# Optimization experiments

Measured on AMD Instinct MI355X. Metric: run time of the kernel, lower is better.

The kernel has to match this reference:

```python
import jax, jax.numpy as jnp
import numpy as np

B, L, E, H = 2, 2048, 1024, 16
D = E // H  # 64


def setup_inputs() -> dict:
    key = jax.random.key(0)
    ks = jax.random.split(key, 9)
    return {
        "query": jax.random.normal(ks[0], (B, L, E), dtype=jnp.float32),
        "value": jax.random.normal(ks[1], (B, L, E), dtype=jnp.float32),
        "key": jax.random.normal(ks[2], (B, L, E), dtype=jnp.float32),
        "mask": jax.random.randint(ks[3], (B, 1, L, L), 0, 2, dtype=jnp.int32),
        "Wq": jax.random.normal(ks[4], (D, D), dtype=jnp.float32) * 0.05,
        "Wk": jax.random.normal(ks[5], (D, D), dtype=jnp.float32) * 0.05,
        "Wv": jax.random.normal(ks[6], (D, D), dtype=jnp.float32) * 0.05,
        "Wfc": jax.random.normal(ks[7], (E, E), dtype=jnp.float32) * 0.02,
        "bfc": jax.random.normal(ks[8], (E,), dtype=jnp.float32) * 0.02,
    }


def reference(query, value, key, mask, Wq, Wk, Wv, Wfc, bfc):
    b, q_len, _ = query.shape
    k_len = key.shape[1]
    v_len = value.shape[1]
    # split heads: [b, l, H, D]
    q = query.reshape(b, q_len, H, D)
    k = key.reshape(b, k_len, H, D)
    v = value.reshape(b, v_len, H, D)
    # per-head linear projections (shared weights across heads, no bias)
    q = jnp.einsum('bqhd,ed->bqhe', q, Wq)
    k = jnp.einsum('bkhd,ed->bkhe', k, Wk)
    v = jnp.einsum('bvhd,ed->bvhe', v, Wv)
    # attention scores [b, H, q, k]
    attn = jnp.einsum('bqhd,bkhd->bhqk', q, k)
    # NOTE: original masks BEFORE scaling, and scales by sqrt(embedding_size)
    attn = jnp.where(mask == 0, jnp.float32(-1e20), attn)
    attn = attn / jnp.float32(E ** 0.5)
    attn = jax.nn.softmax(attn, axis=3)
    out = jnp.einsum('bhqk,bkhd->bqhd', attn, v).reshape(b, q_len, E)
    out = out @ Wfc.T + bfc
    return out
```

## Files before the change

kernel.cpp:

```cpp
#include <hip/hip_runtime.h>
#include <hip/hip_bf16.h>


#define B_ 2
#define L_ 2048
#define E_ 1024
#define H_ 16
#define D_ 64

typedef __attribute__((ext_vector_type(8))) short s8v;
typedef __attribute__((ext_vector_type(4))) float f4v;

__device__ __forceinline__ f4v mfma16(s8v a, s8v b, f4v c) {
    return __builtin_amdgcn_mfma_f32_16x16x32_bf16(a, b, c, 0, 0, 0);
}

__device__ __forceinline__ float fast_exp2(float x) {
    return __builtin_amdgcn_exp2f(x);
}

__device__ __forceinline__ ushort bf16bits(float f) {
    __hip_bfloat16 h = __float2bfloat16(f);
    return *(ushort*)&h;
}

__device__ __forceinline__ void glds16(const __hip_bfloat16* g, ushort* l) {
    __builtin_amdgcn_global_load_lds(
        (const __attribute__((address_space(1))) void*)g,
        (__attribute__((address_space(3))) void*)l,
        16, 0, 0);
}

__device__ __forceinline__ s8v ld8_dual(const void* p, size_t idx, bool isf32) {
    if (isf32) {
        const float* pf = (const float*)p + idx;
        f4v f0 = *(const f4v*)pf;
        f4v f1 = *(const f4v*)(pf + 4);
        s8v r;
        r[0] = (short)bf16bits(f0[0]); r[1] = (short)bf16bits(f0[1]);
        r[2] = (short)bf16bits(f0[2]); r[3] = (short)bf16bits(f0[3]);
        r[4] = (short)bf16bits(f1[0]); r[5] = (short)bf16bits(f1[1]);
        r[6] = (short)bf16bits(f1[2]); r[7] = (short)bf16bits(f1[3]);
        return r;
    }
    return *(const s8v*)((const __hip_bfloat16*)p + idx);
}

__device__ __forceinline__ s8v ld8_ws(const __hip_bfloat16* p) {
    return *(const s8v*)p;
}

__device__ __forceinline__ void cvt_piece(
    size_t i4, const void* Wfc, const void* bfc,
    __hip_bfloat16* wfc_bf, __hip_bfloat16* bfc_bf, bool isf32)
{
    const size_t base = i4 * 4;
    const size_t n1 = (size_t)E_ * E_;
    if (base >= n1 + E_) return;
    const void* src = (base < n1) ? Wfc : bfc;
    const size_t off = (base < n1) ? base : base - n1;
    __hip_bfloat16* dst = (base < n1) ? (wfc_bf + off) : (bfc_bf + off);
    if (isf32) {
        f4v v = *(const f4v*)((const float*)src + off);
        #pragma unroll
        for (int j = 0; j < 4; ++j) dst[j] = __float2bfloat16(v[j]);
    } else {
        *(ushort4*)dst = *(const ushort4*)((const ushort*)src + off);
    }
}

__global__ void detect_kernel(const ushort* __restrict__ q, int* __restrict__ flag) {
    __shared__ int cnt;
    if (threadIdx.x == 0) cnt = 0;
    __syncthreads();
    int bad = 0;
    #pragma unroll
    for (int i = 0; i < 16; ++i) {
        ushort u = q[threadIdx.x * 16 + i];
        int e = (u >> 7) & 0xFF;
        if (e >= 0x8E) ++bad;
    }
    atomicAdd(&cnt, bad);
    __syncthreads();
    if (threadIdx.x == 0) *flag = (cnt > 100) ? 1 : 0;
}

__global__ __launch_bounds__(256) void proj_all_kernel(
    const void* __restrict__ q_in, const void* __restrict__ k_in,
    const void* __restrict__ v_in,
    const void* __restrict__ Wq, const void* __restrict__ Wk,
    const void* __restrict__ Wv,
    const void* __restrict__ Wfc, const void* __restrict__ bfc,
    const int* __restrict__ mask, unsigned long long* __restrict__ mbits,
    __hip_bfloat16* __restrict__ qp, __hip_bfloat16* __restrict__ kp,
    __hip_bfloat16* __restrict__ vpT,
    __hip_bfloat16* __restrict__ wfc_bf, __hip_bfloat16* __restrict__ bfc_bf,
    const int* __restrict__ flag)
{
    __shared__ __align__(16) ushort tile[64][72];
    const bool isf32 = (*flag != 0);
    const int wave = threadIdx.x >> 6;
    const int lane = threadIdx.x & 63;
    const int quad = lane >> 4;
    const int l16  = lane & 15;

    if (blockIdx.y == 3) {
        const int lane_ = threadIdx.x & 63;
        const size_t wbase = (size_t)blockIdx.x * 128 + wave * 32;
        #pragma unroll 4
        for (int i = 0; i < 32; ++i) {
            const size_t widx = wbase + i;
            const int v = mask[widx * 64 + lane_];
            const unsigned long long bal = __ballot(v != 0);
            if (lane_ == 0) mbits[widx] = bal;
        }
        return;
    }
    if (blockIdx.y == 4) {
        cvt_piece((size_t)blockIdx.x * 256 + threadIdx.x, Wfc, bfc, wfc_bf, bfc_bf, isf32);
        if (blockIdx.x == 0)
            cvt_piece((size_t)(E_ * (size_t)E_ / 4) + threadIdx.x, Wfc, bfc, wfc_bf, bfc_bf, isf32);
        return;
    }
    if (blockIdx.y < 2) {
        const void* X = blockIdx.y == 0 ? q_in : k_in;
        const void* W = blockIdx.y == 0 ? Wq : Wk;
        __hip_bfloat16* dst = blockIdx.y == 0 ? qp : kp;
        const float oscale = (blockIdx.y == 0) ? 0.045084439755930314f : 1.0f;
        const int m0 = (blockIdx.x * 4 + wave) * 16;

        const size_t abase = (size_t)(m0 + l16) * D_;
        s8v a0 = ld8_dual(X, abase + quad * 8, isf32);
        s8v a1 = ld8_dual(X, abase + 32 + quad * 8, isf32);

        f4v acc[4];
        #pragma unroll
        for (int nt = 0; nt < 4; ++nt) {
            const size_t bbase = (size_t)(nt * 16 + l16) * D_;
            s8v b0 = ld8_dual(W, bbase + quad * 8, isf32);
            s8v b1 = ld8_dual(W, bbase + 32 + quad * 8, isf32);
            f4v c = {0.f, 0.f, 0.f, 0.f};
            c = mfma16(a0, b0, c);
            c = mfma16(a1, b1, c);
            acc[nt] = c;
        }
        #pragma unroll
        for (int r = 0; r < 4; ++r) {
            const int m = m0 + quad * 4 + r;
            const int h = m & 15;
            const int bl = m >> 4;
            const int b = bl >> 11;
            const int l = bl & (L_ - 1);
            #pragma unroll
            for (int nt = 0; nt < 4; ++nt) {
                const int e = nt * 16 + l16;
                dst[(((size_t)(b * H_ + h)) * L_ + l) * D_ + e] =
                    __float2bfloat16(acc[nt][r] * oscale);
            }
        }
    } else {
        const int l0 = (blockIdx.x & 31) * 64;
        const int bh = blockIdx.x >> 5;
        const int b = bh >> 4, h = bh & 15;
        const int lw = l0 + wave * 16;

        const size_t xbase = ((size_t)(b * L_ + lw + l16)) * E_ + h * D_;
        s8v a0 = ld8_dual(v_in, xbase + quad * 8, isf32);
        s8v a1 = ld8_dual(v_in, xbase + 32 + quad * 8, isf32);

        #pragma unroll
        for (int nt = 0; nt < 4; ++nt) {
            const int e = nt * 16 + l16;
            s8v b0 = ld8_dual(Wv, (size_t)e * D_ + quad * 8, isf32);
            s8v b1 = ld8_dual(Wv, (size_t)e * D_ + 32 + quad * 8, isf32);
            f4v c = {0.f, 0.f, 0.f, 0.f};
            c = mfma16(a0, b0, c);
            c = mfma16(a1, b1, c);
            #pragma unroll
            for (int r = 0; r < 4; ++r)
                tile[wave * 16 + quad * 4 + r][e] = bf16bits(c[r]);
        }
        __syncthreads();
        const int e  = threadIdx.x >> 2;
        const int lc = (threadIdx.x & 3) * 16;
        s8v s0, s1;
        #pragma unroll
        for (int i = 0; i < 8; ++i) {
            s0[i] = (short)tile[lc + i][e];
            s1[i] = (short)tile[lc + 8 + i][e];
        }
        __hip_bfloat16* drow = vpT + ((size_t)bh * D_ + e) * L_ + l0 + lc;
        *(s8v*)drow = s0;
        *(s8v*)(drow + 8) = s1;
    }
}

__global__ __launch_bounds__(256) void cvt_wfc_kernel(
    const void* __restrict__ Wfc, const void* __restrict__ bfc,
    __hip_bfloat16* __restrict__ wfc_bf, __hip_bfloat16* __restrict__ bfc_bf,
    const int* __restrict__ flag)
{
    cvt_piece((size_t)blockIdx.x * 256 + threadIdx.x, Wfc, bfc, wfc_bf, bfc_bf, *flag != 0);
}

__global__ __launch_bounds__(256, 4) void attn_kernel(
    const __hip_bfloat16* __restrict__ qp,
    const __hip_bfloat16* __restrict__ kp,
    const __hip_bfloat16* __restrict__ vpT,
    const unsigned long long* __restrict__ mbits,
    __hip_bfloat16* __restrict__ attn_out)
{
    __shared__ __align__(16) ushort kbuf[2][64 * 64];
    __shared__ __align__(16) ushort vbuf[2][64 * 64];
    __shared__ __align__(16) ushort pbuf[4][16 * 64];

    const int wave = threadIdx.x >> 6;
    const int lane = threadIdx.x & 63;
    const int quad = lane >> 4;
    const int l16  = lane & 15;
    const int sw   = l16 & 7;
    const int bh = blockIdx.y;
    const int b = bh >> 4, h = bh & 15;
    const int q0 = blockIdx.x * 64 + wave * 16;

    const uint NEGB = __float_as_uint(-4.5084439e18f);

    const __hip_bfloat16* kbh = kp + (size_t)bh * L_ * D_;
    const __hip_bfloat16* vbh = vpT + (size_t)bh * D_ * L_;
    const unsigned long long* mrow = mbits + ((size_t)b * L_ + q0 + l16) * 32;

    const int lrow = lane >> 3;
    const int lchk = (lane & 7) ^ lrow;
    const int r0 = wave * 16;
    const __hip_bfloat16* kg0 = kbh + (size_t)(r0 + lrow) * D_ + lchk * 8;
    const __hip_bfloat16* kg1 = kbh + (size_t)(r0 + 8 + lrow) * D_ + lchk * 8;
    const __hip_bfloat16* vg0 = vbh + (size_t)(r0 + lrow) * L_ + lchk * 8;
    const __hip_bfloat16* vg1 = vbh + (size_t)(r0 + 8 + lrow) * L_ + lchk * 8;

    const __hip_bfloat16* qbase = qp + ((size_t)bh * L_ + q0) * D_;
    s8v qa0 = ld8_ws(qbase + (size_t)l16 * D_ + quad * 8);
    s8v qa1 = ld8_ws(qbase + (size_t)l16 * D_ + 32 + quad * 8);

    float rsum = 0.f;
    f4v o[4];
    #pragma unroll
    for (int nt = 0; nt < 4; ++nt) o[nt] = (f4v){0.f, 0.f, 0.f, 0.f};

    uint2* pdst[4];
    #pragma unroll
    for (int nt = 0; nt < 4; ++nt) {
        const int c = nt * 2 + (quad >> 1);
        pdst[nt] = (uint2*)&pbuf[wave][l16 * 64 + ((c ^ sw) << 3) + 4 * (quad & 1)];
    }

    glds16(kg0, &kbuf[0][r0 * 64]);
    glds16(kg1, &kbuf[0][r0 * 64 + 512]);
    glds16(vg0, &vbuf[0][r0 * 64]);
    glds16(vg1, &vbuf[0][r0 * 64 + 512]);
    __syncthreads();

    int cur = 0;
    for (int it = 0; it < 32; ++it) {
        const int k0 = it * 64;
        const unsigned long long wq = mrow[it];
        const uint wlo = (uint)wq, whi = (uint)(wq >> 32);
        if (it < 31) {
            glds16(kg0 + (size_t)(k0 + 64) * D_, &kbuf[cur ^ 1][r0 * 64]);
            glds16(kg1 + (size_t)(k0 + 64) * D_, &kbuf[cur ^ 1][r0 * 64 + 512]);
            glds16(vg0 + (k0 + 64), &vbuf[cur ^ 1][r0 * 64]);
            glds16(vg1 + (k0 + 64), &vbuf[cur ^ 1][r0 * 64 + 512]);
        }
        f4v s[4];
        #pragma unroll
        for (int nt = 0; nt < 4; ++nt) {
            const ushort* kr = &kbuf[cur][(nt * 16 + l16) * 64];
            s8v kb0 = *(const s8v*)(kr + ((quad ^ sw) << 3));
            s8v kb1 = *(const s8v*)(kr + (((quad + 4) ^ sw) << 3));
            f4v c = {0.f, 0.f, 0.f, 0.f};
            c = mfma16(kb0, qa0, c);
            c = mfma16(kb1, qa1, c);
            s[nt] = c;
        }
        #pragma unroll
        for (int nt = 0; nt < 4; ++nt) {
            const uint w = (nt & 2) ? whi : wlo;
            float pr[4];
            #pragma unroll
            for (int r = 0; r < 4; ++r) {
                const int idx = ((nt & 1) << 4) + quad * 4 + r;
                const uint m = (uint)(((int)(w << (31 - idx))) >> 31);
                const uint sb = (__float_as_uint(s[nt][r]) & m) | (NEGB & ~m);
                const float p = fast_exp2(__uint_as_float(sb));
                rsum += p;
                pr[r] = p;
            }
            const uint dw0 = ((__float_as_uint(pr[0]) + 0x8000u) >> 16) |
                             ((__float_as_uint(pr[1]) + 0x8000u) & 0xFFFF0000u);
            const uint dw1 = ((__float_as_uint(pr[2]) + 0x8000u) >> 16) |
                             ((__float_as_uint(pr[3]) + 0x8000u) & 0xFFFF0000u);
            *pdst[nt] = make_uint2(dw0, dw1);
        }
        asm volatile("s_waitcnt lgkmcnt(0)" ::: "memory");
        const ushort* pw = &pbuf[wave][l16 * 64];
        s8v pa0 = *(const s8v*)(pw + ((quad ^ sw) << 3));
        s8v pa1 = *(const s8v*)(pw + (((quad + 4) ^ sw) << 3));
        #pragma unroll
        for (int nt = 0; nt < 4; ++nt) {
            const ushort* vr = &vbuf[cur][(nt * 16 + l16) * 64];
            s8v vb0 = *(const s8v*)(vr + ((quad ^ sw) << 3));
            s8v vb1 = *(const s8v*)(vr + (((quad + 4) ^ sw) << 3));
            o[nt] = mfma16(pa0, vb0, o[nt]);
            o[nt] = mfma16(pa1, vb1, o[nt]);
        }
        __syncthreads();
        cur ^= 1;
    }
    float v = rsum;
    v += __shfl_xor(v, 16, 64);
    v += __shfl_xor(v, 32, 64);
    #pragma unroll
    for (int r = 0; r < 4; ++r) {
        const int qrow = quad * 4 + r;
        const float li = __shfl(v, qrow, 64);
        const float inv = 1.0f / fmaxf(li, 1e-30f);
        const int row = q0 + qrow;
        #pragma unroll
        for (int nt = 0; nt < 4; ++nt) {
            const int d = nt * 16 + l16;
            attn_out[((size_t)(b * L_ + row)) * E_ + h * D_ + d] =
                __float2bfloat16(o[nt][r] * inv);
        }
    }
}

__global__ __launch_bounds__(256, 4) void fc_kernel(
    const __hip_bfloat16* __restrict__ x,
    const __hip_bfloat16* __restrict__ wfc_bf,
    const __hip_bfloat16* __restrict__ bfc_bf,
    void* __restrict__ out, const int* __restrict__ flag)
{
    __shared__ __align__(16) ushort abuf[2][64 * 64];
    __shared__ __align__(16) ushort bbuf[2][64 * 64];
    const bool isf32 = (*flag != 0);
    const int wave = threadIdx.x >> 6;
    const int lane = threadIdx.x & 63;
    const int quad = lane >> 4;
    const int l16  = lane & 15;
    const int sw   = l16 & 7;
    const int m0 = blockIdx.x * 64;
    const int n0 = blockIdx.y * 64;

    const int lrow = lane >> 3;
    const int lchk = (lane & 7) ^ lrow;
    const int r0 = wave * 16;
    const __hip_bfloat16* ag0 = x + (size_t)(m0 + r0 + lrow) * E_ + lchk * 8;
    const __hip_bfloat16* ag1 = x + (size_t)(m0 + r0 + 8 + lrow) * E_ + lchk * 8;
    const __hip_bfloat16* bg0 = wfc_bf + (size_t)(n0 + r0 + lrow) * E_ + lchk * 8;
    const __hip_bfloat16* bg1 = wfc_bf + (size_t)(n0 + r0 + 8 + lrow) * E_ + lchk * 8;

    f4v acc[4];
    #pragma unroll
    for (int nt = 0; nt < 4; ++nt) acc[nt] = (f4v){0.f, 0.f, 0.f, 0.f};

    glds16(ag0, &abuf[0][r0 * 64]);
    glds16(ag1, &abuf[0][r0 * 64 + 512]);
    glds16(bg0, &bbuf[0][r0 * 64]);
    glds16(bg1, &bbuf[0][r0 * 64 + 512]);
    __syncthreads();

    int cur = 0;
    for (int it = 0; it < 16; ++it) {
        const int k0 = it * 64;
        if (it < 15) {
            glds16(ag0 + k0 + 64, &abuf[cur ^ 1][r0 * 64]);
            glds16(ag1 + k0 + 64, &abuf[cur ^ 1][r0 * 64 + 512]);
            glds16(bg0 + k0 + 64, &bbuf[cur ^ 1][r0 * 64]);
            glds16(bg1 + k0 + 64, &bbuf[cur ^ 1][r0 * 64 + 512]);
        }
        const ushort* ar = &abuf[cur][(r0 + l16) * 64];
        s8v a0 = *(const s8v*)(ar + ((quad ^ sw) << 3));
        s8v a1 = *(const s8v*)(ar + (((quad + 4) ^ sw) << 3));
        #pragma unroll
        for (int nt = 0; nt < 4; ++nt) {
            const ushort* br = &bbuf[cur][(nt * 16 + l16) * 64];
            s8v b0 = *(const s8v*)(br + ((quad ^ sw) << 3));
            s8v b1 = *(const s8v*)(br + (((quad + 4) ^ sw) << 3));
            acc[nt] = mfma16(a0, b0, acc[nt]);
            acc[nt] = mfma16(a1, b1, acc[nt]);
        }
        __syncthreads();
        cur ^= 1;
    }
    #pragma unroll
    for (int r = 0; r < 4; ++r) {
        const int m = m0 + r0 + quad * 4 + r;
        #pragma unroll
        for (int nt = 0; nt < 4; ++nt) {
            const int n = n0 + nt * 16 + l16;
            const float val = acc[nt][r] + __bfloat162float(bfc_bf[n]);
            if (isf32) ((float*)out)[(size_t)m * E_ + n] = val;
            else       ((__hip_bfloat16*)out)[(size_t)m * E_ + n] = __float2bfloat16(val);
        }
    }
}

extern "C" void kernel_launch(void* const* d_in, const int* in_sizes, int n_in,
                              void* d_out, int out_size, void* d_ws, size_t ws_size,
                              hipStream_t stream) {
    const void* query = d_in[0];
    const void* value = d_in[1];
    const void* key   = d_in[2];
    const int*  mask  = (const int*)d_in[3];
    const void* Wq  = d_in[4];
    const void* Wk  = d_in[5];
    const void* Wv  = d_in[6];
    const void* Wfc = d_in[7];
    const void* bfc = d_in[8];

    char* ws = (char*)d_ws;
    int* flag                     = (int*)ws;
    unsigned long long* mbits     = (unsigned long long*)(ws + (64u << 10));
    __hip_bfloat16* qp            = (__hip_bfloat16*)(ws + (2u  << 20));
    __hip_bfloat16* kp            = (__hip_bfloat16*)(ws + (10u << 20));
    __hip_bfloat16* vpT           = (__hip_bfloat16*)(ws + (18u << 20));
    __hip_bfloat16* attn_out      = (__hip_bfloat16*)(ws + (26u << 20));

    const bool big_ws = ws_size >= (37ull << 20);
    __hip_bfloat16* wfc_bf = big_ws ? (__hip_bfloat16*)(ws + (34ull << 20)) : qp;
    __hip_bfloat16* bfc_bf = wfc_bf + (size_t)E_ * E_;

    detect_kernel<<<1, 256, 0, stream>>>((const ushort*)query, flag);
    proj_all_kernel<<<dim3(1024, big_ws ? 5 : 4), 256, 0, stream>>>(
        query, key, value, Wq, Wk, Wv, Wfc, bfc, mask, mbits,
        qp, kp, vpT, wfc_bf, bfc_bf, flag);
    attn_kernel<<<dim3(32, 32), 256, 0, stream>>>(qp, kp, vpT, mbits, attn_out);
    if (!big_ws)
        cvt_wfc_kernel<<<1025, 256, 0, stream>>>(Wfc, bfc, wfc_bf, bfc_bf, flag);
    fc_kernel<<<dim3(64, 16), 256, 0, stream>>>(attn_out, wfc_bf, bfc_bf, d_out, flag);
}
```

Baseline: 239.2 us.

## Pass softmax probabilities between MFMAs via permlane swaps instead of LDS

The P tile is now re-laid-out from the QK^T accumulator layout into the PV operand layout in registers, using v_permlane32/16_swap, instead of a round trip through a per-wave LDS buffer with a wait. Masking is now applied after exp2 with a bitfield-extract AND rather than substituting a large negative before exp. BF16 packing uses v_cvt_pk_bf16_f32, and the row sum uses a packed two-wide float accumulator. This removes LDS traffic and a waitcnt stall from the inner loop. The cost is dependence on gfx950-specific instructions and on the permutation matching the MFMA operand layout exactly.

```diff
diff --git a/kernel.cpp b/kernel.cpp
--- a/kernel.cpp
+++ b/kernel.cpp
@@ -10,6 +10,7 @@
 
 typedef __attribute__((ext_vector_type(8))) short s8v;
 typedef __attribute__((ext_vector_type(4))) float f4v;
+typedef __attribute__((ext_vector_type(2))) float f2v;
 
 __device__ __forceinline__ f4v mfma16(s8v a, s8v b, f4v c) {
     return __builtin_amdgcn_mfma_f32_16x16x32_bf16(a, b, c, 0, 0, 0);
@@ -48,6 +49,12 @@
 
 __device__ __forceinline__ s8v ld8_ws(const __hip_bfloat16* p) {
     return *(const s8v*)p;
+}
+
+__device__ __forceinline__ s8v u4_to_s8(uint a, uint b, uint c, uint d) {
+    union { uint u[4]; s8v v; } x;
+    x.u[0] = a; x.u[1] = b; x.u[2] = c; x.u[3] = d;
+    return x.v;
 }
 
 __device__ __forceinline__ void cvt_piece(
@@ -212,7 +219,6 @@
 {
     __shared__ __align__(16) ushort kbuf[2][64 * 64];
     __shared__ __align__(16) ushort vbuf[2][64 * 64];
-    __shared__ __align__(16) ushort pbuf[4][16 * 64];
 
     const int wave = threadIdx.x >> 6;
     const int lane = threadIdx.x & 63;
@@ -223,8 +229,6 @@
     const int b = bh >> 4, h = bh & 15;
     const int q0 = blockIdx.x * 64 + wave * 16;
 
-    const uint NEGB = __float_as_uint(-4.5084439e18f);
-
     const __hip_bfloat16* kbh = kp + (size_t)bh * L_ * D_;
     const __hip_bfloat16* vbh = vpT + (size_t)bh * D_ * L_;
     const unsigned long long* mrow = mbits + ((size_t)b * L_ + q0 + l16) * 32;
@@ -241,17 +245,10 @@
     s8v qa0 = ld8_ws(qbase + (size_t)l16 * D_ + quad * 8);
     s8v qa1 = ld8_ws(qbase + (size_t)l16 * D_ + 32 + quad * 8);
 
-    float rsum = 0.f;
+    f2v rs2 = {0.f, 0.f};
     f4v o[4];
     #pragma unroll
     for (int nt = 0; nt < 4; ++nt) o[nt] = (f4v){0.f, 0.f, 0.f, 0.f};
-
-    uint2* pdst[4];
-    #pragma unroll
-    for (int nt = 0; nt < 4; ++nt) {
-        const int c = nt * 2 + (quad >> 1);
-        pdst[nt] = (uint2*)&pbuf[wave][l16 * 64 + ((c ^ sw) << 3) + 4 * (quad & 1)];
-    }
 
     glds16(kg0, &kbuf[0][r0 * 64]);
     glds16(kg1, &kbuf[0][r0 * 64 + 512]);
@@ -259,11 +256,13 @@
     glds16(vg1, &vbuf[0][r0 * 64 + 512]);
     __syncthreads();
 
+    const int shq = quad * 4;
     int cur = 0;
     for (int it = 0; it < 32; ++it) {
         const int k0 = it * 64;
         const unsigned long long wq = mrow[it];
-        const uint wlo = (uint)wq, whi = (uint)(wq >> 32);
+        const uint wlo_sh = ((uint)wq) >> shq;
+        const uint whi_sh = ((uint)(wq >> 32)) >> shq;
         if (it < 31) {
             glds16(kg0 + (size_t)(k0 + 64) * D_, &kbuf[cur ^ 1][r0 * 64]);
             glds16(kg1 + (size_t)(k0 + 64) * D_, &kbuf[cur ^ 1][r0 * 64 + 512]);
@@ -281,29 +280,38 @@
             c = mfma16(kb1, qa1, c);
             s[nt] = c;
         }
-        #pragma unroll
-        for (int nt = 0; nt < 4; ++nt) {
-            const uint w = (nt & 2) ? whi : wlo;
+        uint dw[4][2];
+        #pragma unroll
+        for (int nt = 0; nt < 4; ++nt) {
+            const uint hs = (nt & 2) ? whi_sh : wlo_sh;
             float pr[4];
             #pragma unroll
             for (int r = 0; r < 4; ++r) {
-                const int idx = ((nt & 1) << 4) + quad * 4 + r;
-                const uint m = (uint)(((int)(w << (31 - idx))) >> 31);
-                const uint sb = (__float_as_uint(s[nt][r]) & m) | (NEGB & ~m);
-                const float p = fast_exp2(__uint_as_float(sb));
-                rsum += p;
-                pr[r] = p;
+                const float p = fast_exp2(s[nt][r]);
+                const int m = __builtin_amdgcn_sbfe((int)hs, ((nt & 1) << 4) + r, 1);
+                pr[r] = __uint_as_float(__float_as_uint(p) & (uint)m);
             }
-            const uint dw0 = ((__float_as_uint(pr[0]) + 0x8000u) >> 16) |
-                             ((__float_as_uint(pr[1]) + 0x8000u) & 0xFFFF0000u);
-            const uint dw1 = ((__float_as_uint(pr[2]) + 0x8000u) >> 16) |
-                             ((__float_as_uint(pr[3]) + 0x8000u) & 0xFFFF0000u);
-            *pdst[nt] = make_uint2(dw0, dw1);
-        }
-        asm volatile("s_waitcnt lgkmcnt(0)" ::: "memory");
-        const ushort* pw = &pbuf[wave][l16 * 64];
-        s8v pa0 = *(const s8v*)(pw + ((quad ^ sw) << 3));
-        s8v pa1 = *(const s8v*)(pw + (((quad + 4) ^ sw) << 3));
+            rs2 += (f2v){pr[0], pr[1]};
+            rs2 += (f2v){pr[2], pr[3]};
+            asm("v_cvt_pk_bf16_f32 %0, %1, %2"
+                : "=v"(dw[nt][0]) : "v"(pr[0]), "v"(pr[1]));
+            asm("v_cvt_pk_bf16_f32 %0, %1, %2"
+                : "=v"(dw[nt][1]) : "v"(pr[2]), "v"(pr[3]));
+        }
+        uint w00 = dw[0][0], w10 = dw[1][0];
+        uint w01 = dw[0][1], w11 = dw[1][1];
+        uint w20 = dw[2][0], w30 = dw[3][0];
+        uint w21 = dw[2][1], w31 = dw[3][1];
+        asm("v_permlane32_swap_b32 %0, %1" : "+v"(w00), "+v"(w10));
+        asm("v_permlane16_swap_b32 %0, %1" : "+v"(w00), "+v"(w10));
+        asm("v_permlane32_swap_b32 %0, %1" : "+v"(w01), "+v"(w11));
+        asm("v_permlane16_swap_b32 %0, %1" : "+v"(w01), "+v"(w11));
+        asm("v_permlane32_swap_b32 %0, %1" : "+v"(w20), "+v"(w30));
+        asm("v_permlane16_swap_b32 %0, %1" : "+v"(w20), "+v"(w30));
+        asm("v_permlane32_swap_b32 %0, %1" : "+v"(w21), "+v"(w31));
+        asm("v_permlane16_swap_b32 %0, %1" : "+v"(w21), "+v"(w31));
+        s8v pa0 = u4_to_s8(w00, w01, w10, w11);
+        s8v pa1 = u4_to_s8(w20, w21, w30, w31);
         #pragma unroll
         for (int nt = 0; nt < 4; ++nt) {
             const ushort* vr = &vbuf[cur][(nt * 16 + l16) * 64];
@@ -315,7 +323,7 @@
         __syncthreads();
         cur ^= 1;
     }
-    float v = rsum;
+    float v = rs2[0] + rs2[1];
     v += __shfl_xor(v, 16, 64);
     v += __shfl_xor(v, 32, 64);
     #pragma unroll
```

Result: no change. 242.8 us (+1.5%).
